# Kernel tuning notes

Measured on AMD Instinct MI355X. Metric: run time of the kernel, lower is better.

Reference implementation:

```python
import jax, jax.numpy as jnp
import numpy as np


def setup_inputs() -> dict:
    key = jax.random.key(0)
    ks = jax.random.split(key, 8)
    B, S, D, U = 32, 2048, 1024, 1024
    sc = 1.0 / np.sqrt(D)
    return {
        "query": jax.random.normal(ks[0], (B, D), dtype=jnp.float32),
        "values": jax.random.normal(ks[1], (B, S, D), dtype=jnp.float32),
        "mask": jax.random.randint(ks[2], (B, S), 0, 2, dtype=jnp.int32),
        "w1": jax.random.normal(ks[3], (D, U), dtype=jnp.float32) * sc,
        "b1": jnp.zeros((U,), dtype=jnp.float32),
        "w2": jax.random.normal(ks[4], (D, U), dtype=jnp.float32) * sc,
        "b2": jnp.zeros((U,), dtype=jnp.float32),
        "v": jax.random.normal(ks[5], (U, 1), dtype=jnp.float32) * (1.0 / np.sqrt(U)),
        "bv": jnp.zeros((1,), dtype=jnp.float32),
    }


def reference(query, values, mask, w1, b1, w2, b2, v, bv):
    # query: [B, D], values: [B, S, D], mask: [B, S]
    q_proj = (query @ w1 + b1)[:, None, :]            # [B, 1, U]
    v_proj = jnp.einsum('bsd,du->bsu', values, w2) + b2  # [B, S, U]
    score = jnp.tanh(q_proj + v_proj) @ v + bv        # [B, S, 1]
    m = mask.astype(score.dtype)[:, :, None]          # [B, S, 1]
    score = score + (1.0 - m) * -1e9
    attention_weights = jax.nn.softmax(score, axis=1)  # [B, S, 1]
    context_vector = jnp.sum(attention_weights * values, axis=1)  # [B, D]
    return context_vector, attention_weights
```

## Files before the change

### kernel.cpp

```cpp
#include <hip/hip_runtime.h>
#include <cstdint>

typedef unsigned short u16;
typedef __bf16 bf16x8 __attribute__((ext_vector_type(8)));
typedef float f32x4 __attribute__((ext_vector_type(4)));
typedef u16 u16x8 __attribute__((ext_vector_type(8)));

#define B_DIM 32
#define S_DIM 2048
#define D_DIM 1024
#define U_DIM 1024
#define M_TOT (B_DIM * S_DIM)

__device__ __forceinline__ u16 f2bf(float f) {
    union { float f; uint32_t u; } a; a.f = f;
    uint32_t u = a.u;
    uint32_t r = (u + 0x7FFFu + ((u >> 16) & 1u)) >> 16;
    return (u16)r;
}
__device__ __forceinline__ float bf2f(u16 h) {
    union { uint32_t u; float f; } a; a.u = ((uint32_t)h) << 16;
    return a.f;
}
__device__ __forceinline__ float fast_tanh(float x) {
    float ax = fabsf(x);
    float e  = __expf(-2.0f * ax);
    float th = __fdividef(1.0f - e, 1.0f + e);
    return copysignf(th, x);
}
__device__ __forceinline__ void gload_lds16(const void* g, void* l) {
    __builtin_amdgcn_global_load_lds(
        (__attribute__((address_space(1))) void*)(uintptr_t)g,
        (__attribute__((address_space(3))) void*)(uint32_t)(uintptr_t)l,
        16, 0, 0);
}

__global__ void build_index_kernel(const int* __restrict__ mask, int* __restrict__ idx,
                                   int* __restrict__ cnt) {
    const int b = blockIdx.x, t = threadIdx.x;
    __shared__ int wsum[4];
    const int base = t * 8;
    int m[8]; int c = 0;
#pragma unroll
    for (int i = 0; i < 8; ++i) { m[i] = mask[b * S_DIM + base + i] != 0; c += m[i]; }
    const int lane = t & 63, w = t >> 6;
    int pre = c;
    for (int o = 1; o < 64; o <<= 1) { int v = __shfl_up(pre, o); if (lane >= o) pre += v; }
    if (lane == 63) wsum[w] = pre;
    __syncthreads();
    int woff = 0;
    for (int i = 0; i < w; ++i) woff += wsum[i];
    int excl = woff + pre - c;
#pragma unroll
    for (int i = 0; i < 8; ++i) if (m[i]) idx[b * S_DIM + excl++] = base + i;
    if (t == 255) cnt[b] = woff + pre;
}

__global__ void convert_masked_kernel(const float* __restrict__ values, u16* __restrict__ vbf,
                                      const int* __restrict__ idx, const int* __restrict__ cnt) {
    const int b = blockIdx.x, c = blockIdx.y, t = threadIdx.x;
    const int cb = cnt[b];
    const int* ib = idx + b * S_DIM;
    for (int ii = c; ii < cb; ii += 64) {
        const int s = ib[ii];
        const float4* src = (const float4*)(values + ((size_t)b * S_DIM + s) * D_DIM) + t;
        ushort4* dst = (ushort4*)(vbf + ((size_t)b * S_DIM + s) * D_DIM) + t;
        float4 v = *src;
        ushort4 o;
        o.x = f2bf(v.x); o.y = f2bf(v.y); o.z = f2bf(v.z); o.w = f2bf(v.w);
        *dst = o;
    }
}

__global__ void transpose_w2_kernel(const float* __restrict__ w2, u16* __restrict__ w2t) {
    __shared__ float tile[32][33];
    int bx = blockIdx.x * 32, by = blockIdx.y * 32;
    int tx = threadIdx.x, ty = threadIdx.y;
    for (int i = 0; i < 32; i += 8)
        tile[ty + i][tx] = w2[(size_t)(by + ty + i) * U_DIM + bx + tx];
    __syncthreads();
    for (int i = 0; i < 32; i += 8)
        w2t[(size_t)(bx + ty + i) * D_DIM + by + tx] = f2bf(tile[tx][ty + i]);
}

__global__ void qproj_kernel(const float* __restrict__ q, const float* __restrict__ w1,
                             const float* __restrict__ b1, const float* __restrict__ b2,
                             float* __restrict__ qpb) {
    const int b = blockIdx.x, uc = blockIdx.y;
    const int u0 = uc * 32;
    const int ul = threadIdx.x & 31;
    const int dg = threadIdx.x >> 5;
    __shared__ float ql[D_DIM];
    __shared__ float red[8][32];
    for (int d = threadIdx.x; d < D_DIM; d += 256) ql[d] = q[b * D_DIM + d];
    __syncthreads();
    float acc = 0.f;
    const int d0 = dg * 128;
    for (int d = d0; d < d0 + 128; ++d)
        acc += ql[d] * w1[(size_t)d * U_DIM + u0 + ul];
    red[dg][ul] = acc;
    __syncthreads();
    if (threadIdx.x < 32) {
        float s = b1[u0 + ul] + b2[u0 + ul];
#pragma unroll
        for (int g = 0; g < 8; ++g) s += red[g][ul];
        qpb[b * U_DIM + u0 + ul] = s;
    }
}

__global__ __launch_bounds__(512, 2)
void score_gemm8_kernel(const u16* __restrict__ vbf, const u16* __restrict__ w2t,
                        const float* __restrict__ qpb, const float* __restrict__ vvec,
                        const int* __restrict__ idx, const int* __restrict__ cnt,
                        float* __restrict__ spart) {
    const int p    = blockIdx.x;
    const int xcd  = p & 7;
    const int slot = p >> 3;
    const int mt   = xcd * 32 + (slot >> 2);
    const int nt   = slot & 3;
    const int bb   = mt >> 3;
    const int lm   = mt & 7;
    const int n0   = nt * 256;

    const int cnt_b = cnt[bb];
    if (lm * 256 >= cnt_b) return;

    __shared__ __align__(16) __bf16 Abuf[2][256 * 64];
    __shared__ __align__(16) __bf16 Bbuf[2][256 * 64];
    __shared__ float qv_lds[256], vv_lds[256];
    __shared__ float red[4][256];

    const int tid  = threadIdx.x;
    const int lane = tid & 63;
    const int wid  = tid >> 6;
    const int wm   = wid >> 2;
    const int wn   = wid & 3;

    if (tid < 256) qv_lds[tid] = qpb[bb * U_DIM + n0 + tid];
    else           vv_lds[tid - 256] = vvec[n0 + (tid - 256)];

    const int tr = tid >> 3;
    const int sc = (((tid & 7) ^ (tr & 7)) << 3);
    const int* ib = idx + bb * S_DIM;
    const u16* vb_base = vbf + (size_t)bb * S_DIM * D_DIM + sc;
    size_t arow_off[4];
#pragma unroll
    for (int j = 0; j < 4; ++j) {
        int cp = lm * 256 + tr + j * 64;
        cp = cp < cnt_b ? cp : cnt_b - 1;
        arow_off[j] = (size_t)ib[cp] * D_DIM;
    }
    const u16* bsrc = w2t + (size_t)(n0 + tr) * D_DIM + sc;

#pragma unroll
    for (int j = 0; j < 4; ++j) {
        gload_lds16(vb_base + arow_off[j], &Abuf[0][j * 4096 + tid * 8]);
        gload_lds16(bsrc + (size_t)j * 64 * D_DIM, &Bbuf[0][j * 4096 + tid * 8]);
    }

    f32x4 acc[8][4];
#pragma unroll
    for (int mi = 0; mi < 8; ++mi)
#pragma unroll
        for (int nj = 0; nj < 4; ++nj) acc[mi][nj] = (f32x4){0.f, 0.f, 0.f, 0.f};

    const int colL = lane & 15;
    const int grp  = lane >> 4;
    const int xork = (lane & 7) << 3;
    const int kix0 = (grp * 8) ^ xork;
    const int kix1 = ((32 + grp * 8)) ^ xork;
    const int arow = wm * 128 + colL;
    const int brow = wn * 64 + colL;

    bf16x8 aR[4], bR[4];

    for (int t = 0; t < 16; ++t) {
        const int cur = t & 1, nxt = cur ^ 1;
        const __bf16* Ac = Abuf[cur];
        const __bf16* Bc = Bbuf[cur];
        const size_t kofs = (size_t)(t + 1) * 64;

        asm volatile("s_waitcnt vmcnt(0)" ::: "memory");
        __builtin_amdgcn_s_barrier();
        __builtin_amdgcn_sched_barrier(0);

#pragma unroll
        for (int mi = 0; mi < 4; ++mi) aR[mi] = *(const bf16x8*)&Ac[(arow + mi * 16) * 64 + kix0];
#pragma unroll
        for (int nj = 0; nj < 4; ++nj) bR[nj] = *(const bf16x8*)&Bc[(brow + nj * 16) * 64 + kix0];
        if (t < 15) {
            gload_lds16(vb_base + arow_off[0] + kofs, &Abuf[nxt][tid * 8]);
            gload_lds16(vb_base + arow_off[1] + kofs, &Abuf[nxt][4096 + tid * 8]);
        }
        __builtin_amdgcn_s_setprio(1);
#pragma unroll
        for (int mi = 0; mi < 4; ++mi)
#pragma unroll
            for (int nj = 0; nj < 4; ++nj)
                acc[mi][nj] = __builtin_amdgcn_mfma_f32_16x16x32_bf16(aR[mi], bR[nj], acc[mi][nj], 0, 0, 0);
        __builtin_amdgcn_s_setprio(0);

#pragma unroll
        for (int mi = 0; mi < 4; ++mi) aR[mi] = *(const bf16x8*)&Ac[(arow + 64 + mi * 16) * 64 + kix0];
        if (t < 15) {
            gload_lds16(vb_base + arow_off[2] + kofs, &Abuf[nxt][2 * 4096 + tid * 8]);
            gload_lds16(vb_base + arow_off[3] + kofs, &Abuf[nxt][3 * 4096 + tid * 8]);
        }
        __builtin_amdgcn_sched_barrier(0);
        __builtin_amdgcn_s_barrier();
        __builtin_amdgcn_s_setprio(1);
#pragma unroll
        for (int mi = 0; mi < 4; ++mi)
#pragma unroll
            for (int nj = 0; nj < 4; ++nj)
                acc[mi + 4][nj] = __builtin_amdgcn_mfma_f32_16x16x32_bf16(aR[mi], bR[nj], acc[mi + 4][nj], 0, 0, 0);
        __builtin_amdgcn_s_setprio(0);

#pragma unroll
        for (int mi = 0; mi < 4; ++mi) aR[mi] = *(const bf16x8*)&Ac[(arow + mi * 16) * 64 + kix1];
#pragma unroll
        for (int nj = 0; nj < 4; ++nj) bR[nj] = *(const bf16x8*)&Bc[(brow + nj * 16) * 64 + kix1];
        if (t < 15) {
            gload_lds16(bsrc + kofs,                   &Bbuf[nxt][tid * 8]);
            gload_lds16(bsrc + kofs + (size_t)65536,   &Bbuf[nxt][4096 + tid * 8]);
        }
        __builtin_amdgcn_sched_barrier(0);
        __builtin_amdgcn_s_barrier();
        __builtin_amdgcn_s_setprio(1);
#pragma unroll
        for (int mi = 0; mi < 4; ++mi)
#pragma unroll
            for (int nj = 0; nj < 4; ++nj)
                acc[mi][nj] = __builtin_amdgcn_mfma_f32_16x16x32_bf16(aR[mi], bR[nj], acc[mi][nj], 0, 0, 0);
        __builtin_amdgcn_s_setprio(0);

#pragma unroll
        for (int mi = 0; mi < 4; ++mi) aR[mi] = *(const bf16x8*)&Ac[(arow + 64 + mi * 16) * 64 + kix1];
        if (t < 15) {
            gload_lds16(bsrc + kofs + (size_t)2 * 65536, &Bbuf[nxt][2 * 4096 + tid * 8]);
            gload_lds16(bsrc + kofs + (size_t)3 * 65536, &Bbuf[nxt][3 * 4096 + tid * 8]);
        }
        __builtin_amdgcn_sched_barrier(0);
        __builtin_amdgcn_s_barrier();
        __builtin_amdgcn_s_setprio(1);
#pragma unroll
        for (int mi = 0; mi < 4; ++mi)
#pragma unroll
            for (int nj = 0; nj < 4; ++nj)
                acc[mi + 4][nj] = __builtin_amdgcn_mfma_f32_16x16x32_bf16(aR[mi], bR[nj], acc[mi + 4][nj], 0, 0, 0);
        __builtin_amdgcn_s_setprio(0);
    }

    float rs[8][4];
#pragma unroll
    for (int mi = 0; mi < 8; ++mi)
#pragma unroll
        for (int r = 0; r < 4; ++r) rs[mi][r] = 0.f;

#pragma unroll
    for (int nj = 0; nj < 4; ++nj) {
        const int cl = wn * 64 + nj * 16 + colL;
        const float qadd = qv_lds[cl];
        const float vmul = vv_lds[cl];
#pragma unroll
        for (int mi = 0; mi < 8; ++mi)
#pragma unroll
            for (int r = 0; r < 4; ++r)
                rs[mi][r] += fast_tanh(acc[mi][nj][r] + qadd) * vmul;
    }
#pragma unroll
    for (int mi = 0; mi < 8; ++mi)
#pragma unroll
        for (int r = 0; r < 4; ++r) {
            float s = rs[mi][r];
            s += __shfl_xor(s, 1); s += __shfl_xor(s, 2);
            s += __shfl_xor(s, 4); s += __shfl_xor(s, 8);
            if (colL == 0) red[wn][wm * 128 + mi * 16 + grp * 4 + r] = s;
        }
    __syncthreads();
    if (tid < 256) {
        const int cp = lm * 256 + tid;
        if (cp < cnt_b) {
            const int orig = ib[cp];
            spart[(size_t)nt * M_TOT + bb * S_DIM + orig] =
                red[0][tid] + red[1][tid] + red[2][tid] + red[3][tid];
        }
    }
}

__global__ __launch_bounds__(256)
void score_fallback_kernel(const float* __restrict__ values, const float* __restrict__ w2,
                           const float* __restrict__ qpb, const float* __restrict__ vvec,
                           float* __restrict__ spart) {
    int row0 = blockIdx.x * 16;
    int b = row0 >> 11;
    __shared__ float vr[16][D_DIM];
    for (int i = threadIdx.x; i < 16 * D_DIM; i += 256)
        vr[i >> 10][i & 1023] = values[(size_t)row0 * D_DIM + i];
    __syncthreads();
    float rs[16];
#pragma unroll
    for (int r = 0; r < 16; ++r) rs[r] = 0.f;
    for (int uu = threadIdx.x; uu < U_DIM; uu += 256) {
        float acc[16];
#pragma unroll
        for (int r = 0; r < 16; ++r) acc[r] = 0.f;
        for (int d = 0; d < D_DIM; ++d) {
            float wv = w2[(size_t)d * U_DIM + uu];
#pragma unroll
            for (int r = 0; r < 16; ++r) acc[r] += vr[r][d] * wv;
        }
        float qv = qpb[b * U_DIM + uu], vu = vvec[uu];
#pragma unroll
        for (int r = 0; r < 16; ++r) rs[r] += fast_tanh(acc[r] + qv) * vu;
    }
#pragma unroll
    for (int r = 0; r < 16; ++r) {
        float s = rs[r];
        for (int o = 1; o < 64; o <<= 1) s += __shfl_xor(s, o);
        rs[r] = s;
    }
    __shared__ float wred[16][4];
    int lane = threadIdx.x & 63, wid = threadIdx.x >> 6;
    if (lane == 0)
        for (int r = 0; r < 16; ++r) wred[r][wid] = rs[r];
    __syncthreads();
    if (threadIdx.x < 16)
        spart[row0 + threadIdx.x] = wred[threadIdx.x][0] + wred[threadIdx.x][1] +
                                    wred[threadIdx.x][2] + wred[threadIdx.x][3];
}

__global__ void softmax_kernel(const float* __restrict__ spart, const int* __restrict__ mask,
                               float* __restrict__ wout, int nparts) {
    int b = blockIdx.x, t = threadIdx.x;
    float sc[8]; int mk[8];
    float mx = -1e30f;
#pragma unroll
    for (int i = 0; i < 8; ++i) {
        int s = t + i * 256;
        mk[i] = mask[b * S_DIM + s];
        float vsum = 0.f;
        if (mk[i])
            for (int p = 0; p < nparts; ++p) vsum += spart[(size_t)p * M_TOT + b * S_DIM + s];
        sc[i] = vsum;
        if (mk[i]) mx = fmaxf(mx, vsum);
    }
    for (int o = 1; o < 64; o <<= 1) mx = fmaxf(mx, __shfl_xor(mx, o));
    __shared__ float red[4], red2[4];
    if ((t & 63) == 0) red[t >> 6] = mx;
    __syncthreads();
    mx = fmaxf(fmaxf(red[0], red[1]), fmaxf(red[2], red[3]));
    float sum = 0.f, ev[8];
#pragma unroll
    for (int i = 0; i < 8; ++i) {
        ev[i] = mk[i] ? __expf(sc[i] - mx) : 0.f;
        sum += ev[i];
    }
    for (int o = 1; o < 64; o <<= 1) sum += __shfl_xor(sum, o);
    if ((t & 63) == 0) red2[t >> 6] = sum;
    __syncthreads();
    sum = red2[0] + red2[1] + red2[2] + red2[3];
    float inv = 1.0f / sum;
#pragma unroll
    for (int i = 0; i < 8; ++i) wout[b * S_DIM + t + i * 256] = ev[i] * inv;
}

__global__ void ctx_partial_kernel(const u16* __restrict__ vbf, const float* __restrict__ w,
                                   const int* __restrict__ idx, const int* __restrict__ cnt,
                                   float* __restrict__ part) {
    const int b = blockIdx.x, c = blockIdx.y, t = threadIdx.x;
    const int cb = cnt[b];
    const int* ib = idx + b * S_DIM;
    const u16* vb0 = vbf + (size_t)b * S_DIM * D_DIM + t * 8;
    float acc[8];
#pragma unroll
    for (int i = 0; i < 8; ++i) acc[i] = 0.f;
    for (int ii = c; ii < cb; ii += 32) {
        const int s = ib[ii];
        const float wv = w[b * S_DIM + s];
        u16x8 vv = *(const u16x8*)(vb0 + (size_t)s * D_DIM);
#pragma unroll
        for (int i = 0; i < 8; ++i) acc[i] += wv * bf2f(vv[i]);
    }
    float* pp = part + ((size_t)b * 32 + c) * D_DIM + t * 8;
#pragma unroll
    for (int i = 0; i < 8; ++i) pp[i] = acc[i];
}
__global__ void ctx_partial_f32_kernel(const float* __restrict__ values, const float* __restrict__ w,
                                       float* __restrict__ part) {
    int b = blockIdx.x, c = blockIdx.y, t = threadIdx.x;
    const float4* vb = (const float4*)(values + ((size_t)b * S_DIM + c * 256) * D_DIM) + t;
    const float* wb = w + b * S_DIM + c * 256;
    float a0 = 0, a1 = 0, a2 = 0, a3 = 0;
    for (int s = 0; s < 256; ++s) {
        float wv = wb[s];
        float4 vv = vb[(size_t)s * 256];
        a0 += wv * vv.x; a1 += wv * vv.y; a2 += wv * vv.z; a3 += wv * vv.w;
    }
    float* pp = part + ((size_t)b * 8 + c) * D_DIM + t * 4;
    pp[0] = a0; pp[1] = a1; pp[2] = a2; pp[3] = a3;
}

__global__ void ctx_reduce_kernel(const float* __restrict__ part, float* __restrict__ out, int nchunks) {
    int b = blockIdx.x, t = threadIdx.x;
    for (int d = t; d < D_DIM; d += 256) {
        float s = 0.f;
        for (int c = 0; c < nchunks; ++c) s += part[((size_t)b * nchunks + c) * D_DIM + d];
        out[b * D_DIM + d] = s;
    }
}

extern "C" void kernel_launch(void* const* d_in, const int* in_sizes, int n_in,
                              void* d_out, int out_size, void* d_ws, size_t ws_size,
                              hipStream_t stream) {
    const float* query  = (const float*)d_in[0];
    const float* values = (const float*)d_in[1];
    const int*   mask   = (const int*)d_in[2];
    const float* w1     = (const float*)d_in[3];
    const float* b1     = (const float*)d_in[4];
    const float* w2     = (const float*)d_in[5];
    const float* b2     = (const float*)d_in[6];
    const float* v      = (const float*)d_in[7];

    float* out  = (float*)d_out;
    float* wout = out + B_DIM * D_DIM;
    char* ws = (char*)d_ws;

    const size_t SZ_VBF = (size_t)M_TOT * D_DIM * 2;
    const size_t SZ_W2T = (size_t)U_DIM * D_DIM * 2;
    const size_t SZ_QPB = (size_t)B_DIM * U_DIM * 4;
    const size_t SZ_SPART = (size_t)8 * M_TOT * 4;
    const size_t SZ_PART  = (size_t)B_DIM * 32 * D_DIM * 4;
    const size_t SZ_IDX   = (size_t)M_TOT * 4 + 4096;
    const size_t need = SZ_VBF + SZ_W2T + SZ_QPB + SZ_SPART + SZ_PART + SZ_IDX;

    if (ws_size >= need) {
        u16*   vbf   = (u16*)ws;
        u16*   w2t   = (u16*)(ws + SZ_VBF);
        float* qpb   = (float*)(ws + SZ_VBF + SZ_W2T);
        float* spart = (float*)(ws + SZ_VBF + SZ_W2T + SZ_QPB);
        float* part  = (float*)(ws + SZ_VBF + SZ_W2T + SZ_QPB + SZ_SPART);
        int*   idx   = (int*)(ws + SZ_VBF + SZ_W2T + SZ_QPB + SZ_SPART + SZ_PART);
        int*   cnt   = idx + M_TOT;

        build_index_kernel<<<32, 256, 0, stream>>>(mask, idx, cnt);
        convert_masked_kernel<<<dim3(32, 64), 256, 0, stream>>>(values, vbf, idx, cnt);
        transpose_w2_kernel<<<dim3(32, 32), dim3(32, 8), 0, stream>>>(w2, w2t);
        qproj_kernel<<<dim3(32, 32), 256, 0, stream>>>(query, w1, b1, b2, qpb);
        score_gemm8_kernel<<<1024, 512, 0, stream>>>(vbf, w2t, qpb, v, idx, cnt, spart);
        softmax_kernel<<<32, 256, 0, stream>>>(spart, mask, wout, 4);
        ctx_partial_kernel<<<dim3(32, 32), 128, 0, stream>>>(vbf, wout, idx, cnt, part);
        ctx_reduce_kernel<<<32, 256, 0, stream>>>(part, out, 32);
    } else {
        float* qpb   = (float*)ws;
        float* spart = (float*)(ws + SZ_QPB);
        float* part  = (float*)(ws + SZ_QPB + (size_t)M_TOT * 4);
        qproj_kernel<<<dim3(32, 32), 256, 0, stream>>>(query, w1, b1, b2, qpb);
        score_fallback_kernel<<<4096, 256, 0, stream>>>(values, w2, qpb, v, spart);
        softmax_kernel<<<32, 256, 0, stream>>>(spart, mask, wout, 1);
        ctx_partial_f32_kernel<<<dim3(32, 8), 256, 0, stream>>>(values, wout, part);
        ctx_reduce_kernel<<<32, 256, 0, stream>>>(part, out, 8);
    }
}
```

Measured before the change: 227.5 us.

## Shrink score GEMM tiles to 128x128 and merge prep kernels into one launch

The score GEMM changes from 256x256 tiles with 512 threads to 128x128 tiles with 256 threads. This gives 4096 blocks over 8 N-slices, so masked-out tail tiles are skipped at finer granularity and occupancy and load balance improve. The cost is lower operand reuse per block and more partial-score slices for softmax to sum. Separately, index building, the query projection and the w2 transpose are fused into one prep kernel to cut launch overhead.

```diff
diff --git a/kernel.cpp b/kernel.cpp
--- a/kernel.cpp
+++ b/kernel.cpp
@@ -35,25 +35,64 @@
         16, 0, 0);
 }
 
-__global__ void build_index_kernel(const int* __restrict__ mask, int* __restrict__ idx,
-                                   int* __restrict__ cnt) {
-    const int b = blockIdx.x, t = threadIdx.x;
-    __shared__ int wsum[4];
-    const int base = t * 8;
-    int m[8]; int c = 0;
-#pragma unroll
-    for (int i = 0; i < 8; ++i) { m[i] = mask[b * S_DIM + base + i] != 0; c += m[i]; }
-    const int lane = t & 63, w = t >> 6;
-    int pre = c;
-    for (int o = 1; o < 64; o <<= 1) { int v = __shfl_up(pre, o); if (lane >= o) pre += v; }
-    if (lane == 63) wsum[w] = pre;
-    __syncthreads();
-    int woff = 0;
-    for (int i = 0; i < w; ++i) woff += wsum[i];
-    int excl = woff + pre - c;
-#pragma unroll
-    for (int i = 0; i < 8; ++i) if (m[i]) idx[b * S_DIM + excl++] = base + i;
-    if (t == 255) cnt[b] = woff + pre;
+__global__ void prep_kernel(const int* __restrict__ mask, int* __restrict__ idx, int* __restrict__ cnt,
+                            const float* __restrict__ q, const float* __restrict__ w1,
+                            const float* __restrict__ b1, const float* __restrict__ b2,
+                            float* __restrict__ qpb,
+                            const float* __restrict__ w2, u16* __restrict__ w2t) {
+    const int bid = blockIdx.x;
+    const int t = threadIdx.x;
+    if (bid < 32) {
+        const int b = bid;
+        __shared__ int wsum[4];
+        const int base = t * 8;
+        int m[8]; int c = 0;
+#pragma unroll
+        for (int i = 0; i < 8; ++i) { m[i] = mask[b * S_DIM + base + i] != 0; c += m[i]; }
+        const int lane = t & 63, w = t >> 6;
+        int pre = c;
+        for (int o = 1; o < 64; o <<= 1) { int v = __shfl_up(pre, o); if (lane >= o) pre += v; }
+        if (lane == 63) wsum[w] = pre;
+        __syncthreads();
+        int woff = 0;
+        for (int i = 0; i < w; ++i) woff += wsum[i];
+        int excl = woff + pre - c;
+#pragma unroll
+        for (int i = 0; i < 8; ++i) if (m[i]) idx[b * S_DIM + excl++] = base + i;
+        if (t == 255) cnt[b] = woff + pre;
+    } else if (bid < 1056) {
+        const int qb = bid - 32;
+        const int b = qb >> 5, uc = qb & 31;
+        const int u0 = uc * 32;
+        const int ul = t & 31;
+        const int dg = t >> 5;
+        __shared__ float ql[D_DIM];
+        __shared__ float redq[8][32];
+        for (int d = t; d < D_DIM; d += 256) ql[d] = q[b * D_DIM + d];
+        __syncthreads();
+        float acc = 0.f;
+        const int d0 = dg * 128;
+        for (int d = d0; d < d0 + 128; ++d)
+            acc += ql[d] * w1[(size_t)d * U_DIM + u0 + ul];
+        redq[dg][ul] = acc;
+        __syncthreads();
+        if (t < 32) {
+            float s = b1[u0 + ul] + b2[u0 + ul];
+#pragma unroll
+            for (int g = 0; g < 8; ++g) s += redq[g][ul];
+            qpb[b * U_DIM + u0 + ul] = s;
+        }
+    } else {
+        const int tq = bid - 1056;
+        const int bx = (tq >> 5) * 32, by = (tq & 31) * 32;
+        const int tx = t & 31, ty = t >> 5;
+        __shared__ float tile[32][33];
+        for (int i = 0; i < 32; i += 8)
+            tile[ty + i][tx] = w2[(size_t)(by + ty + i) * U_DIM + bx + tx];
+        __syncthreads();
+        for (int i = 0; i < 32; i += 8)
+            w2t[(size_t)(bx + ty + i) * D_DIM + by + tx] = f2bf(tile[tx][ty + i]);
+    }
 }
 
 __global__ void convert_masked_kernel(const float* __restrict__ values, u16* __restrict__ vbf,
@@ -72,15 +111,149 @@
     }
 }
 
-__global__ void transpose_w2_kernel(const float* __restrict__ w2, u16* __restrict__ w2t) {
-    __shared__ float tile[32][33];
-    int bx = blockIdx.x * 32, by = blockIdx.y * 32;
-    int tx = threadIdx.x, ty = threadIdx.y;
-    for (int i = 0; i < 32; i += 8)
-        tile[ty + i][tx] = w2[(size_t)(by + ty + i) * U_DIM + bx + tx];
-    __syncthreads();
-    for (int i = 0; i < 32; i += 8)
-        w2t[(size_t)(bx + ty + i) * D_DIM + by + tx] = f2bf(tile[tx][ty + i]);
+__global__ __launch_bounds__(256, 2)
+void score_gemm4_kernel(const u16* __restrict__ vbf, const u16* __restrict__ w2t,
+                        const float* __restrict__ qpb, const float* __restrict__ vvec,
+                        const int* __restrict__ idx, const int* __restrict__ cnt,
+                        float* __restrict__ spart) {
+    const int p    = blockIdx.x;
+    const int xcd  = p & 7;
+    const int slot = p >> 3;
+    const int g    = xcd * 512 + slot;
+    const int bb   = g >> 7;
+    const int rem  = g & 127;
+    const int lm   = rem >> 3;
+    const int nt   = rem & 7;
+    const int n0   = nt * 128;
+
+    const int cnt_b = cnt[bb];
+    if (lm * 128 >= cnt_b) return;
+
+    __shared__ __align__(16) __bf16 Abuf[2][128 * 64];
+    __shared__ __align__(16) __bf16 Bbuf[2][128 * 64];
+    __shared__ float qv_lds[128], vv_lds[128];
+    __shared__ float red[2][128];
+
+    const int tid  = threadIdx.x;
+    const int lane = tid & 63;
+    const int wid  = tid >> 6;
+    const int wm   = wid >> 1;
+    const int wn   = wid & 1;
+
+    if (tid < 128) qv_lds[tid] = qpb[bb * U_DIM + n0 + tid];
+    else           vv_lds[tid - 128] = vvec[n0 + (tid - 128)];
+
+    const int tr = tid >> 3;
+    const int sc = (((tid & 7) ^ (tr & 7)) << 3);
+    const int* ib = idx + bb * S_DIM;
+    const u16* vb_base = vbf + (size_t)bb * S_DIM * D_DIM + sc;
+    size_t arow_off[4];
+#pragma unroll
+    for (int j = 0; j < 4; ++j) {
+        int cp = lm * 128 + tr + j * 32;
+        cp = cp < cnt_b ? cp : cnt_b - 1;
+        arow_off[j] = (size_t)ib[cp] * D_DIM;
+    }
+    const u16* bsrc = w2t + (size_t)(n0 + tr) * D_DIM + sc;
+
+#pragma unroll
+    for (int j = 0; j < 4; ++j) {
+        gload_lds16(vb_base + arow_off[j], &Abuf[0][j * 2048 + tid * 8]);
+        gload_lds16(bsrc + (size_t)j * 32 * D_DIM, &Bbuf[0][j * 2048 + tid * 8]);
+    }
+
+    f32x4 acc[4][4];
+#pragma unroll
+    for (int mi = 0; mi < 4; ++mi)
+#pragma unroll
+        for (int nj = 0; nj < 4; ++nj) acc[mi][nj] = (f32x4){0.f, 0.f, 0.f, 0.f};
+
+    const int colL = lane & 15;
+    const int grp  = lane >> 4;
+    const int xork = (lane & 7) << 3;
+    const int kix0 = (grp * 8) ^ xork;
+    const int kix1 = ((32 + grp * 8)) ^ xork;
+    const int arow = wm * 64 + colL;
+    const int brow = wn * 64 + colL;
+
+    bf16x8 aR[4], bR[4];
+
+    for (int t = 0; t < 16; ++t) {
+        const int cur = t & 1, nxt = cur ^ 1;
+        const __bf16* Ac = Abuf[cur];
+        const __bf16* Bc = Bbuf[cur];
+        const size_t kofs = (size_t)(t + 1) * 64;
+
+        asm volatile("s_waitcnt vmcnt(0)" ::: "memory");
+        __builtin_amdgcn_s_barrier();
+        __builtin_amdgcn_sched_barrier(0);
+
+#pragma unroll
+        for (int mi = 0; mi < 4; ++mi) aR[mi] = *(const bf16x8*)&Ac[(arow + mi * 16) * 64 + kix0];
+#pragma unroll
+        for (int nj = 0; nj < 4; ++nj) bR[nj] = *(const bf16x8*)&Bc[(brow + nj * 16) * 64 + kix0];
+        if (t < 15) {
+#pragma unroll
+            for (int j = 0; j < 4; ++j) {
+                gload_lds16(vb_base + arow_off[j] + kofs, &Abuf[nxt][j * 2048 + tid * 8]);
+                gload_lds16(bsrc + kofs + (size_t)j * 32 * D_DIM, &Bbuf[nxt][j * 2048 + tid * 8]);
+            }
+        }
+        __builtin_amdgcn_s_setprio(1);
+#pragma unroll
+        for (int mi = 0; mi < 4; ++mi)
+#pragma unroll
+            for (int nj = 0; nj < 4; ++nj)
+                acc[mi][nj] = __builtin_amdgcn_mfma_f32_16x16x32_bf16(aR[mi], bR[nj], acc[mi][nj], 0, 0, 0);
+        __builtin_amdgcn_s_setprio(0);
+
+#pragma unroll
+        for (int mi = 0; mi < 4; ++mi) aR[mi] = *(const bf16x8*)&Ac[(arow + mi * 16) * 64 + kix1];
+#pragma unroll
+        for (int nj = 0; nj < 4; ++nj) bR[nj] = *(const bf16x8*)&Bc[(brow + nj * 16) * 64 + kix1];
+        __builtin_amdgcn_s_setprio(1);
+#pragma unroll
+        for (int mi = 0; mi < 4; ++mi)
+#pragma unroll
+            for (int nj = 0; nj < 4; ++nj)
+                acc[mi][nj] = __builtin_amdgcn_mfma_f32_16x16x32_bf16(aR[mi], bR[nj], acc[mi][nj], 0, 0, 0);
+        __builtin_amdgcn_s_setprio(0);
+    }
+
+    float rs[4][4];
+#pragma unroll
+    for (int mi = 0; mi < 4; ++mi)
+#pragma unroll
+        for (int r = 0; r < 4; ++r) rs[mi][r] = 0.f;
+
+#pragma unroll
+    for (int nj = 0; nj < 4; ++nj) {
+        const int cl = wn * 64 + nj * 16 + colL;
+        const float qadd = qv_lds[cl];
+        const float vmul = vv_lds[cl];
+#pragma unroll
+        for (int mi = 0; mi < 4; ++mi)
+#pragma unroll
+            for (int r = 0; r < 4; ++r)
+                rs[mi][r] += fast_tanh(acc[mi][nj][r] + qadd) * vmul;
+    }
+#pragma unroll
+    for (int mi = 0; mi < 4; ++mi)
+#pragma unroll
+        for (int r = 0; r < 4; ++r) {
+            float s = rs[mi][r];
+            s += __shfl_xor(s, 1); s += __shfl_xor(s, 2);
+            s += __shfl_xor(s, 4); s += __shfl_xor(s, 8);
+            if (colL == 0) red[wn][wm * 64 + mi * 16 + grp * 4 + r] = s;
+        }
+    __syncthreads();
+    if (tid < 128) {
+        const int cp = lm * 128 + tid;
+        if (cp < cnt_b) {
+            const int orig = ib[cp];
+            spart[(size_t)nt * M_TOT + bb * S_DIM + orig] = red[0][tid] + red[1][tid];
+        }
+    }
 }
 
 __global__ void qproj_kernel(const float* __restrict__ q, const float* __restrict__ w1,
@@ -91,200 +264,20 @@
     const int ul = threadIdx.x & 31;
     const int dg = threadIdx.x >> 5;
     __shared__ float ql[D_DIM];
-    __shared__ float red[8][32];
+    __shared__ float redq[8][32];
     for (int d = threadIdx.x; d < D_DIM; d += 256) ql[d] = q[b * D_DIM + d];
     __syncthreads();
     float acc = 0.f;
     const int d0 = dg * 128;
     for (int d = d0; d < d0 + 128; ++d)
         acc += ql[d] * w1[(size_t)d * U_DIM + u0 + ul];
-    red[dg][ul] = acc;
+    redq[dg][ul] = acc;
     __syncthreads();
     if (threadIdx.x < 32) {
         float s = b1[u0 + ul] + b2[u0 + ul];
 #pragma unroll
-        for (int g = 0; g < 8; ++g) s += red[g][ul];
+        for (int g = 0; g < 8; ++g) s += redq[g][ul];
         qpb[b * U_DIM + u0 + ul] = s;
-    }
-}
-
-__global__ __launch_bounds__(512, 2)
-void score_gemm8_kernel(const u16* __restrict__ vbf, const u16* __restrict__ w2t,
-                        const float* __restrict__ qpb, const float* __restrict__ vvec,
-                        const int* __restrict__ idx, const int* __restrict__ cnt,
-                        float* __restrict__ spart) {
-    const int p    = blockIdx.x;
-    const int xcd  = p & 7;
-    const int slot = p >> 3;
-    const int mt   = xcd * 32 + (slot >> 2);
-    const int nt   = slot & 3;
-    const int bb   = mt >> 3;
-    const int lm   = mt & 7;
-    const int n0   = nt * 256;
-
-    const int cnt_b = cnt[bb];
-    if (lm * 256 >= cnt_b) return;
-
-    __shared__ __align__(16) __bf16 Abuf[2][256 * 64];
-    __shared__ __align__(16) __bf16 Bbuf[2][256 * 64];
-    __shared__ float qv_lds[256], vv_lds[256];
-    __shared__ float red[4][256];
-
-    const int tid  = threadIdx.x;
-    const int lane = tid & 63;
-    const int wid  = tid >> 6;
-    const int wm   = wid >> 2;
-    const int wn   = wid & 3;
-
-    if (tid < 256) qv_lds[tid] = qpb[bb * U_DIM + n0 + tid];
-    else           vv_lds[tid - 256] = vvec[n0 + (tid - 256)];
-
-    const int tr = tid >> 3;
-    const int sc = (((tid & 7) ^ (tr & 7)) << 3);
-    const int* ib = idx + bb * S_DIM;
-    const u16* vb_base = vbf + (size_t)bb * S_DIM * D_DIM + sc;
-    size_t arow_off[4];
-#pragma unroll
-    for (int j = 0; j < 4; ++j) {
-        int cp = lm * 256 + tr + j * 64;
-        cp = cp < cnt_b ? cp : cnt_b - 1;
-        arow_off[j] = (size_t)ib[cp] * D_DIM;
-    }
-    const u16* bsrc = w2t + (size_t)(n0 + tr) * D_DIM + sc;
-
-#pragma unroll
-    for (int j = 0; j < 4; ++j) {
-        gload_lds16(vb_base + arow_off[j], &Abuf[0][j * 4096 + tid * 8]);
-        gload_lds16(bsrc + (size_t)j * 64 * D_DIM, &Bbuf[0][j * 4096 + tid * 8]);
-    }
-
-    f32x4 acc[8][4];
-#pragma unroll
-    for (int mi = 0; mi < 8; ++mi)
-#pragma unroll
-        for (int nj = 0; nj < 4; ++nj) acc[mi][nj] = (f32x4){0.f, 0.f, 0.f, 0.f};
-
-    const int colL = lane & 15;
-    const int grp  = lane >> 4;
-    const int xork = (lane & 7) << 3;
-    const int kix0 = (grp * 8) ^ xork;
-    const int kix1 = ((32 + grp * 8)) ^ xork;
-    const int arow = wm * 128 + colL;
-    const int brow = wn * 64 + colL;
-
-    bf16x8 aR[4], bR[4];
-
-    for (int t = 0; t < 16; ++t) {
-        const int cur = t & 1, nxt = cur ^ 1;
-        const __bf16* Ac = Abuf[cur];
-        const __bf16* Bc = Bbuf[cur];
-        const size_t kofs = (size_t)(t + 1) * 64;
-
-        asm volatile("s_waitcnt vmcnt(0)" ::: "memory");
-        __builtin_amdgcn_s_barrier();
-        __builtin_amdgcn_sched_barrier(0);
-
-#pragma unroll
-        for (int mi = 0; mi < 4; ++mi) aR[mi] = *(const bf16x8*)&Ac[(arow + mi * 16) * 64 + kix0];
-#pragma unroll
-        for (int nj = 0; nj < 4; ++nj) bR[nj] = *(const bf16x8*)&Bc[(brow + nj * 16) * 64 + kix0];
-        if (t < 15) {
-            gload_lds16(vb_base + arow_off[0] + kofs, &Abuf[nxt][tid * 8]);
-            gload_lds16(vb_base + arow_off[1] + kofs, &Abuf[nxt][4096 + tid * 8]);
-        }
-        __builtin_amdgcn_s_setprio(1);
-#pragma unroll
-        for (int mi = 0; mi < 4; ++mi)
-#pragma unroll
-            for (int nj = 0; nj < 4; ++nj)
-                acc[mi][nj] = __builtin_amdgcn_mfma_f32_16x16x32_bf16(aR[mi], bR[nj], acc[mi][nj], 0, 0, 0);
-        __builtin_amdgcn_s_setprio(0);
-
-#pragma unroll
-        for (int mi = 0; mi < 4; ++mi) aR[mi] = *(const bf16x8*)&Ac[(arow + 64 + mi * 16) * 64 + kix0];
-        if (t < 15) {
-            gload_lds16(vb_base + arow_off[2] + kofs, &Abuf[nxt][2 * 4096 + tid * 8]);
-            gload_lds16(vb_base + arow_off[3] + kofs, &Abuf[nxt][3 * 4096 + tid * 8]);
-        }
-        __builtin_amdgcn_sched_barrier(0);
-        __builtin_amdgcn_s_barrier();
-        __builtin_amdgcn_s_setprio(1);
-#pragma unroll
-        for (int mi = 0; mi < 4; ++mi)
-#pragma unroll
-            for (int nj = 0; nj < 4; ++nj)
-                acc[mi + 4][nj] = __builtin_amdgcn_mfma_f32_16x16x32_bf16(aR[mi], bR[nj], acc[mi + 4][nj], 0, 0, 0);
-        __builtin_amdgcn_s_setprio(0);
-
-#pragma unroll
-        for (int mi = 0; mi < 4; ++mi) aR[mi] = *(const bf16x8*)&Ac[(arow + mi * 16) * 64 + kix1];
-#pragma unroll
-        for (int nj = 0; nj < 4; ++nj) bR[nj] = *(const bf16x8*)&Bc[(brow + nj * 16) * 64 + kix1];
-        if (t < 15) {
-            gload_lds16(bsrc + kofs,                   &Bbuf[nxt][tid * 8]);
-            gload_lds16(bsrc + kofs + (size_t)65536,   &Bbuf[nxt][4096 + tid * 8]);
-        }
-        __builtin_amdgcn_sched_barrier(0);
-        __builtin_amdgcn_s_barrier();
-        __builtin_amdgcn_s_setprio(1);
-#pragma unroll
-        for (int mi = 0; mi < 4; ++mi)
-#pragma unroll
-            for (int nj = 0; nj < 4; ++nj)
-                acc[mi][nj] = __builtin_amdgcn_mfma_f32_16x16x32_bf16(aR[mi], bR[nj], acc[mi][nj], 0, 0, 0);
-        __builtin_amdgcn_s_setprio(0);
-
-#pragma unroll
-        for (int mi = 0; mi < 4; ++mi) aR[mi] = *(const bf16x8*)&Ac[(arow + 64 + mi * 16) * 64 + kix1];
-        if (t < 15) {
-            gload_lds16(bsrc + kofs + (size_t)2 * 65536, &Bbuf[nxt][2 * 4096 + tid * 8]);
-            gload_lds16(bsrc + kofs + (size_t)3 * 65536, &Bbuf[nxt][3 * 4096 + tid * 8]);
-        }
-        __builtin_amdgcn_sched_barrier(0);
-        __builtin_amdgcn_s_barrier();
-        __builtin_amdgcn_s_setprio(1);
-#pragma unroll
-        for (int mi = 0; mi < 4; ++mi)
-#pragma unroll
-            for (int nj = 0; nj < 4; ++nj)
-                acc[mi + 4][nj] = __builtin_amdgcn_mfma_f32_16x16x32_bf16(aR[mi], bR[nj], acc[mi + 4][nj], 0, 0, 0);
-        __builtin_amdgcn_s_setprio(0);
-    }
-
-    float rs[8][4];
-#pragma unroll
-    for (int mi = 0; mi < 8; ++mi)
-#pragma unroll
-        for (int r = 0; r < 4; ++r) rs[mi][r] = 0.f;
-
-#pragma unroll
-    for (int nj = 0; nj < 4; ++nj) {
-        const int cl = wn * 64 + nj * 16 + colL;
-        const float qadd = qv_lds[cl];
-        const float vmul = vv_lds[cl];
-#pragma unroll
-        for (int mi = 0; mi < 8; ++mi)
-#pragma unroll
-            for (int r = 0; r < 4; ++r)
-                rs[mi][r] += fast_tanh(acc[mi][nj][r] + qadd) * vmul;
-    }
-#pragma unroll
-    for (int mi = 0; mi < 8; ++mi)
-#pragma unroll
-        for (int r = 0; r < 4; ++r) {
-            float s = rs[mi][r];
-            s += __shfl_xor(s, 1); s += __shfl_xor(s, 2);
-            s += __shfl_xor(s, 4); s += __shfl_xor(s, 8);
-            if (colL == 0) red[wn][wm * 128 + mi * 16 + grp * 4 + r] = s;
-        }
-    __syncthreads();
-    if (tid < 256) {
-        const int cp = lm * 256 + tid;
-        if (cp < cnt_b) {
-            const int orig = ib[cp];
-            spart[(size_t)nt * M_TOT + bb * S_DIM + orig] =
-                red[0][tid] + red[1][tid] + red[2][tid] + red[3][tid];
-        }
     }
 }
 
@@ -443,12 +436,10 @@
         int*   idx   = (int*)(ws + SZ_VBF + SZ_W2T + SZ_QPB + SZ_SPART + SZ_PART);
         int*   cnt   = idx + M_TOT;
 
-        build_index_kernel<<<32, 256, 0, stream>>>(mask, idx, cnt);
+        prep_kernel<<<2080, 256, 0, stream>>>(mask, idx, cnt, query, w1, b1, b2, qpb, w2, w2t);
         convert_masked_kernel<<<dim3(32, 64), 256, 0, stream>>>(values, vbf, idx, cnt);
-        transpose_w2_kernel<<<dim3(32, 32), dim3(32, 8), 0, stream>>>(w2, w2t);
-        qproj_kernel<<<dim3(32, 32), 256, 0, stream>>>(query, w1, b1, b2, qpb);
-        score_gemm8_kernel<<<1024, 512, 0, stream>>>(vbf, w2t, qpb, v, idx, cnt, spart);
-        softmax_kernel<<<32, 256, 0, stream>>>(spart, mask, wout, 4);
+        score_gemm4_kernel<<<4096, 256, 0, stream>>>(vbf, w2t, qpb, v, idx, cnt, spart);
+        softmax_kernel<<<32, 256, 0, stream>>>(spart, mask, wout, 8);
         ctx_partial_kernel<<<dim3(32, 32), 128, 0, stream>>>(vbf, wout, idx, cnt, part);
         ctx_reduce_kernel<<<32, 256, 0, stream>>>(part, out, 32);
     } else {
```

Result: faster. 217.9 us (median of 2 runs) (-4.2%).
